# Kernel optimization log

Measured on AMD Instinct MI355X. Metric: run time of the kernel, lower is better.

Reference implementation:

```python
import jax, jax.numpy as jnp
import numpy as np

E = 400000
N = 100000
B = 64
D = 128          # token_dim
H = 128          # hidden_dim
A = 2 * H        # action_dim


def setup_inputs() -> dict:
    key = jax.random.key(0)
    ks = jax.random.split(key, 12)
    inp = {
        "relation_tokens": jax.random.normal(ks[0], (E, D), jnp.float32),
        "node_tokens": jax.random.normal(ks[1], (N, D), jnp.float32),
        "edge_index": jax.random.randint(ks[2], (2, E), 0, N, jnp.int64 if jax.config.jax_enable_x64 else jnp.int32),
        "question_tokens": jax.random.normal(ks[3], (B, D), jnp.float32),
        "edge_batch": jax.random.randint(ks[4], (E,), 0, B, jnp.int64 if jax.config.jax_enable_x64 else jnp.int32),
        # learned params (xavier-like small init); stored as [in, out] for x @ W
        "W_rel": jax.random.normal(ks[5], (D, H), jnp.float32) * 0.05,
        "W_node": jax.random.normal(ks[6], (D, H), jnp.float32) * 0.05,
        "W_qgate": jax.random.normal(ks[7], (D, A), jnp.float32) * 0.05,
        "W_mlp1": jax.random.normal(ks[8], (A, A), jnp.float32) * 0.05,
        "b_mlp1": jnp.zeros((A,), jnp.float32),
        "W_mlp2": jax.random.normal(ks[9], (A, A), jnp.float32) * 0.05,
        "b_mlp2": jnp.zeros((A,), jnp.float32),
    }
    return inp


def reference(relation_tokens, node_tokens, edge_index, question_tokens, edge_batch,
              W_rel, W_node, W_qgate, W_mlp1, b_mlp1, W_mlp2, b_mlp2):
    # TrajectoryAgent.precompute_action_keys (dropout=0 -> identity)
    tail_nodes = edge_index[1]                       # [E]
    tail_tokens = node_tokens[tail_nodes]            # gather -> [E, D]
    q_tokens = question_tokens[edge_batch]           # gather -> [E, D]

    rel_key = relation_tokens @ W_rel                # [E, H]
    node_key = tail_tokens @ W_node                  # [E, H]
    q_gate = jax.nn.sigmoid(q_tokens @ W_qgate)      # [E, 2H]

    action_key = jnp.concatenate((rel_key, node_key), axis=-1) * q_gate  # [E, 2H]

    # action_mlp: Linear -> exact GELU -> Linear (torch nn.GELU default = erf)
    h = jax.nn.gelu(action_key @ W_mlp1 + b_mlp1, approximate=False)
    return h @ W_mlp2 + b_mlp2                       # [E, 2H]
```

## Files before the change

### kernel.cpp

```cpp
#include <hip/hip_runtime.h>

typedef __bf16 bf16;
typedef bf16 bf16x4 __attribute__((ext_vector_type(4)));
typedef bf16 bf16x8 __attribute__((ext_vector_type(8)));
typedef float f32x4 __attribute__((ext_vector_type(4)));

#define WS_PK1   0
#define WS_PK2   32768
#define WS_PK3   98304
#define WS_QG_F  163840

__global__ void prep_weights(const float* __restrict__ Wrel,
                             const float* __restrict__ Wnode,
                             const float* __restrict__ W1,
                             const float* __restrict__ W2,
                             bf16* __restrict__ ws) {
  int id = blockIdx.x * 256 + threadIdx.x;
  if (id < 32768) {
    int cg = id >> 13, rem = id & 8191;
    int kk = rem >> 11;
    int ai = (rem >> 9) & 3;
    int l  = (rem >> 3) & 63;
    int j  = rem & 7;
    int n  = (cg & 1) * 64 + ai * 16 + (l & 15);
    int k  = kk * 32 + (l >> 4) * 8 + j;
    const float* src = (cg >> 1) ? Wnode : Wrel;
    ws[WS_PK1 + id] = (bf16)src[k * 128 + n];
  } else if (id < 98304) {
    int t = id - 32768;
    int cg = t >> 14, rem = t & 16383;
    int kk = rem >> 11;
    int ai = (rem >> 9) & 3;
    int l  = (rem >> 3) & 63;
    int j  = rem & 7;
    int n  = cg * 64 + ai * 16 + (l & 15);
    int k  = kk * 32 + (l >> 4) * 8 + j;
    ws[WS_PK2 + t] = (bf16)W1[k * 256 + n];
  } else if (id < 163840) {
    int t = id - 98304;
    int cg = t >> 14, rem = t & 16383;
    int kk = rem >> 11;
    int ai = (rem >> 9) & 3;
    int l  = (rem >> 3) & 63;
    int j  = rem & 7;
    int n  = cg * 64 + ai * 16 + (l & 15);
    int k  = kk * 32 + (l >> 4) * 8 + j;
    ws[WS_PK3 + t] = (bf16)W2[k * 256 + n];
  }
}

__global__ void prep_qg(const float* __restrict__ question,
                        const float* __restrict__ Wq,
                        float* __restrict__ qgf) {
  int b = blockIdx.x, c = threadIdx.x;
  float s = 0.f;
#pragma unroll 8
  for (int k = 0; k < 128; ++k) s += question[b * 128 + k] * Wq[k * 256 + c];
  qgf[b * 256 + c] = 1.f / (1.f + expf(-s));
}

__device__ __forceinline__ float gelu_fast(float x) {
  float x2 = x * x;
  float p = fmaf(0.0356774081f, x2, 0.7978845608f);
  float y = p * x;
  float e = __expf(2.f * y);
  float r = __builtin_amdgcn_rcpf(e + 1.f);
  float th = 1.f - 2.f * r;
  return 0.5f * x * (1.f + th);
}

__global__ __launch_bounds__(512, 4) void fused_main(
    const float* __restrict__ rel_tok,
    const float* __restrict__ node_tok,
    const int*   __restrict__ tail_idx,
    const int*   __restrict__ ebatch,
    const bf16*  __restrict__ pk1,
    const bf16*  __restrict__ pk2,
    const bf16*  __restrict__ pk3,
    const float* __restrict__ qgf,
    const float* __restrict__ b1,
    const float* __restrict__ b2,
    float* __restrict__ out)
{
  __shared__ char s_buf[65536];
  __shared__ int  s_eb[128];

  const int tid = threadIdx.x;
  const int w   = tid >> 6;
  const int eh  = w >> 2;
  const int cg  = w & 3;
  const int l   = tid & 63;
  const int lo  = l & 15;
  const int hi  = l >> 4;
  const int base = blockIdx.x * 128;

  if (tid < 128) s_eb[tid] = ebatch[base + tid];

  {
    const float4* g = (const float4*)rel_tok + (size_t)base * 32;
#pragma unroll
    for (int i = 0; i < 8; ++i) {
      int idx = tid + i * 512;
      int row = idx >> 5, c4 = idx & 31;
      float4 v = g[idx];
      bf16x4 b; b[0] = (bf16)v.x; b[1] = (bf16)v.y; b[2] = (bf16)v.z; b[3] = (bf16)v.w;
      int off = row * 256 + ((c4 * 8) ^ ((row & 7) << 4));
      *(bf16x4*)(s_buf + off) = b;
    }
#pragma unroll
    for (int i = 0; i < 8; ++i) {
      int idx = tid + i * 512;
      int row = idx >> 5, c4 = idx & 31;
      int tail = tail_idx[base + row];
      float4 v = ((const float4*)node_tok)[(size_t)tail * 32 + c4];
      bf16x4 b; b[0] = (bf16)v.x; b[1] = (bf16)v.y; b[2] = (bf16)v.z; b[3] = (bf16)v.w;
      int off = 32768 + row * 256 + ((c4 * 8) ^ ((row & 7) << 4));
      *(bf16x4*)(s_buf + off) = b;
    }
  }
  __syncthreads();

  const f32x4 zero4 = {0.f, 0.f, 0.f, 0.f};
  const int h1 = cg >> 1;

  f32x4 acc1[4][4];
#pragma unroll
  for (int ai = 0; ai < 4; ++ai)
#pragma unroll
    for (int bj = 0; bj < 4; ++bj) acc1[ai][bj] = zero4;

  {
    const bf16* pw = pk1 + cg * 8192 + l * 8;
#pragma unroll
    for (int kk = 0; kk < 4; ++kk) {
      bf16x8 a[4];
#pragma unroll
      for (int ai = 0; ai < 4; ++ai)
        a[ai] = *(const bf16x8*)(pw + (kk * 4 + ai) * 512);
#pragma unroll
      for (int bj = 0; bj < 4; ++bj) {
        int e = eh * 64 + bj * 16 + lo;
        bf16x8 b = *(const bf16x8*)(s_buf + h1 * 32768 + e * 256 +
                                    ((kk * 64 + hi * 16) ^ ((e & 7) << 4)));
#pragma unroll
        for (int ai = 0; ai < 4; ++ai)
          acc1[ai][bj] = __builtin_amdgcn_mfma_f32_16x16x32_bf16(a[ai], b, acc1[ai][bj], 0, 0, 0);
      }
    }
  }
  __syncthreads();

#pragma unroll
  for (int bj = 0; bj < 4; ++bj) {
    int e = eh * 64 + bj * 16 + lo;
    int qrow = s_eb[e] * 256;
#pragma unroll
    for (int ai = 0; ai < 4; ++ai) {
      int col0 = cg * 64 + ai * 16 + hi * 4;
      float4 g = *(const float4*)(qgf + qrow + col0);
      bf16x4 pk;
      pk[0] = (bf16)(acc1[ai][bj][0] * g.x);
      pk[1] = (bf16)(acc1[ai][bj][1] * g.y);
      pk[2] = (bf16)(acc1[ai][bj][2] * g.z);
      pk[3] = (bf16)(acc1[ai][bj][3] * g.w);
      int off = e * 512 + ((2 * col0) ^ ((e & 7) << 4));
      *(bf16x4*)(s_buf + off) = pk;
    }
  }
  __syncthreads();

  f32x4 acc2[4][4];
#pragma unroll
  for (int ai = 0; ai < 4; ++ai)
#pragma unroll
    for (int bj = 0; bj < 4; ++bj) acc2[ai][bj] = zero4;

  {
    const bf16* pw = pk2 + cg * 16384 + l * 8;
#pragma unroll
    for (int kk = 0; kk < 8; ++kk) {
      bf16x8 a[4];
#pragma unroll
      for (int ai = 0; ai < 4; ++ai)
        a[ai] = *(const bf16x8*)(pw + (kk * 4 + ai) * 512);
#pragma unroll
      for (int bj = 0; bj < 4; ++bj) {
        int e = eh * 64 + bj * 16 + lo;
        bf16x8 b = *(const bf16x8*)(s_buf + e * 512 +
                                    ((kk * 64 + hi * 16) ^ ((e & 7) << 4)));
#pragma unroll
        for (int ai = 0; ai < 4; ++ai)
          acc2[ai][bj] = __builtin_amdgcn_mfma_f32_16x16x32_bf16(a[ai], b, acc2[ai][bj], 0, 0, 0);
      }
    }
  }
  __syncthreads();

  {
    float4 b1v[4];
#pragma unroll
    for (int ai = 0; ai < 4; ++ai)
      b1v[ai] = *(const float4*)(b1 + cg * 64 + ai * 16 + hi * 4);
#pragma unroll
    for (int bj = 0; bj < 4; ++bj) {
      int e = eh * 64 + bj * 16 + lo;
#pragma unroll
      for (int ai = 0; ai < 4; ++ai) {
        int col0 = cg * 64 + ai * 16 + hi * 4;
        bf16x4 pk;
        pk[0] = (bf16)gelu_fast(acc2[ai][bj][0] + b1v[ai].x);
        pk[1] = (bf16)gelu_fast(acc2[ai][bj][1] + b1v[ai].y);
        pk[2] = (bf16)gelu_fast(acc2[ai][bj][2] + b1v[ai].z);
        pk[3] = (bf16)gelu_fast(acc2[ai][bj][3] + b1v[ai].w);
        int off = e * 512 + ((2 * col0) ^ ((e & 7) << 4));
        *(bf16x4*)(s_buf + off) = pk;
      }
    }
  }
  __syncthreads();

  f32x4 acc3[4][4];
#pragma unroll
  for (int ai = 0; ai < 4; ++ai)
#pragma unroll
    for (int bj = 0; bj < 4; ++bj) acc3[ai][bj] = zero4;

  {
    const bf16* pw = pk3 + cg * 16384 + l * 8;
#pragma unroll
    for (int kk = 0; kk < 8; ++kk) {
      bf16x8 a[4];
#pragma unroll
      for (int ai = 0; ai < 4; ++ai)
        a[ai] = *(const bf16x8*)(pw + (kk * 4 + ai) * 512);
#pragma unroll
      for (int bj = 0; bj < 4; ++bj) {
        int e = eh * 64 + bj * 16 + lo;
        bf16x8 b = *(const bf16x8*)(s_buf + e * 512 +
                                    ((kk * 64 + hi * 16) ^ ((e & 7) << 4)));
#pragma unroll
        for (int ai = 0; ai < 4; ++ai)
          acc3[ai][bj] = __builtin_amdgcn_mfma_f32_16x16x32_bf16(a[ai], b, acc3[ai][bj], 0, 0, 0);
      }
    }
  }

  {
    float4 b2v[4];
#pragma unroll
    for (int ai = 0; ai < 4; ++ai)
      b2v[ai] = *(const float4*)(b2 + cg * 64 + ai * 16 + hi * 4);
#pragma unroll
    for (int bj = 0; bj < 4; ++bj) {
      int e = eh * 64 + bj * 16 + lo;
#pragma unroll
      for (int ai = 0; ai < 4; ++ai) {
        int col0 = cg * 64 + ai * 16 + hi * 4;
        float4 o;
        o.x = acc3[ai][bj][0] + b2v[ai].x;
        o.y = acc3[ai][bj][1] + b2v[ai].y;
        o.z = acc3[ai][bj][2] + b2v[ai].z;
        o.w = acc3[ai][bj][3] + b2v[ai].w;
        *(float4*)(out + (size_t)(base + e) * 256 + col0) = o;
      }
    }
  }
}

extern "C" void kernel_launch(void* const* d_in, const int* in_sizes, int n_in,
                              void* d_out, int out_size, void* d_ws, size_t ws_size,
                              hipStream_t stream) {
  const float* rel    = (const float*)d_in[0];
  const float* node   = (const float*)d_in[1];
  const int*   eidx   = (const int*)d_in[2];
  const float* quest  = (const float*)d_in[3];
  const int*   ebat   = (const int*)d_in[4];
  const float* Wrel   = (const float*)d_in[5];
  const float* Wnode  = (const float*)d_in[6];
  const float* Wq     = (const float*)d_in[7];
  const float* W1     = (const float*)d_in[8];
  const float* bias1  = (const float*)d_in[9];
  const float* W2     = (const float*)d_in[10];
  const float* bias2  = (const float*)d_in[11];
  float* outp = (float*)d_out;
  bf16* ws = (bf16*)d_ws;
  float* qgf = (float*)(ws + WS_QG_F);

  const int E = in_sizes[4];

  prep_weights<<<640, 256, 0, stream>>>(Wrel, Wnode, W1, W2, ws);
  prep_qg<<<64, 256, 0, stream>>>(quest, Wq, qgf);
  fused_main<<<E / 128, 512, 0, stream>>>(
      rel, node, eidx + E, ebat,
      ws + WS_PK1, ws + WS_PK2, ws + WS_PK3, qgf,
      bias1, bias2, outp);
}
```

Before: 317.7 us.

## Stream weights into LDS via async global_load_lds double buffer, smaller 64-edge tiles

Weight fragments for all three GEMMs are now staged into a double-buffered LDS region with global_load_lds, two steps ahead, synchronised by manual vmcnt/lgkmcnt waits and raw barriers. Before, each wave read them straight from global memory inside the MFMA loops. The block shrinks to 256 threads and 64 edges with launch bounds (256,2), and the XOR swizzle widens to 16 rows. The question gate is stored in bf16 and prefetched into registers early, together with the biases and edge-batch indices. This is meant to hide weight-load latency behind MFMA work, at the cost of fragile hand-written wait counts and lower occupancy per CU.

```diff
diff --git a/kernel.cpp b/kernel.cpp
--- a/kernel.cpp
+++ b/kernel.cpp
@@ -8,7 +8,7 @@
 #define WS_PK1   0
 #define WS_PK2   32768
 #define WS_PK3   98304
-#define WS_QG_F  163840
+#define WS_QG    163840
 
 __global__ void prep_weights(const float* __restrict__ Wrel,
                              const float* __restrict__ Wnode,
@@ -51,12 +51,12 @@
 
 __global__ void prep_qg(const float* __restrict__ question,
                         const float* __restrict__ Wq,
-                        float* __restrict__ qgf) {
+                        bf16* __restrict__ qg) {
   int b = blockIdx.x, c = threadIdx.x;
   float s = 0.f;
 #pragma unroll 8
   for (int k = 0; k < 128; ++k) s += question[b * 128 + k] * Wq[k * 256 + c];
-  qgf[b * 256 + c] = 1.f / (1.f + expf(-s));
+  qg[b * 256 + c] = (bf16)(1.f / (1.f + expf(-s)));
 }
 
 __device__ __forceinline__ float gelu_fast(float x) {
@@ -69,7 +69,15 @@
   return 0.5f * x * (1.f + th);
 }
 
-__global__ __launch_bounds__(512, 4) void fused_main(
+typedef __attribute__((address_space(1))) const void gq_t;
+typedef __attribute__((address_space(3))) void lq_t;
+#define GLD16(g, s) __builtin_amdgcn_global_load_lds((gq_t*)(g), (lq_t*)(s), 16, 0, 0)
+#define WAIT_VM4()   { asm volatile("s_waitcnt vmcnt(4)" ::: "memory"); __builtin_amdgcn_sched_barrier(0); }
+#define WAIT_VM0()   { asm volatile("s_waitcnt vmcnt(0)" ::: "memory"); __builtin_amdgcn_sched_barrier(0); }
+#define WAIT_LGKM0() { asm volatile("s_waitcnt lgkmcnt(0)" ::: "memory"); __builtin_amdgcn_sched_barrier(0); }
+#define BAR() __builtin_amdgcn_s_barrier()
+
+__global__ __launch_bounds__(256, 2) void fused_main(
     const float* __restrict__ rel_tok,
     const float* __restrict__ node_tok,
     const int*   __restrict__ tail_idx,
@@ -77,51 +85,79 @@
     const bf16*  __restrict__ pk1,
     const bf16*  __restrict__ pk2,
     const bf16*  __restrict__ pk3,
-    const float* __restrict__ qgf,
+    const bf16*  __restrict__ qg,
     const float* __restrict__ b1,
     const float* __restrict__ b2,
     float* __restrict__ out)
 {
-  __shared__ char s_buf[65536];
-  __shared__ int  s_eb[128];
+  __shared__ char s_buf[32768];
+  __shared__ char s_w[32768];
 
   const int tid = threadIdx.x;
-  const int w   = tid >> 6;
-  const int eh  = w >> 2;
-  const int cg  = w & 3;
+  const int cg  = tid >> 6;
   const int l   = tid & 63;
   const int lo  = l & 15;
   const int hi  = l >> 4;
-  const int base = blockIdx.x * 128;
-
-  if (tid < 128) s_eb[tid] = ebatch[base + tid];
+  const int base = blockIdx.x * 64;
+  const int h1  = cg >> 1;
+
+  auto issue_step = [&](int s) {
+    const bf16* g;
+    if (s < 4)       g = pk1 + cg * 8192  + s * 2048;
+    else if (s < 12) g = pk2 + cg * 16384 + (s - 4) * 2048;
+    else             g = pk3 + cg * 16384 + (s - 12) * 2048;
+    g += l * 8;
+    char* d = s_w + (s & 1) * 16384 + cg * 4096;
+#pragma unroll
+    for (int ai = 0; ai < 4; ++ai) GLD16(g + ai * 512, d + ai * 1024);
+  };
+
+  issue_step(0);
+  issue_step(1);
+
+  float4 b1v[4], b2v[4];
+#pragma unroll
+  for (int ai = 0; ai < 4; ++ai) {
+    b1v[ai] = *(const float4*)(b1 + cg * 64 + ai * 16 + hi * 4);
+    b2v[ai] = *(const float4*)(b2 + cg * 64 + ai * 16 + hi * 4);
+  }
+  int ebv[4];
+#pragma unroll
+  for (int bj = 0; bj < 4; ++bj) ebv[bj] = ebatch[base + bj * 16 + lo];
+  bf16x4 gv[4][4];
+#pragma unroll
+  for (int bj = 0; bj < 4; ++bj)
+#pragma unroll
+    for (int ai = 0; ai < 4; ++ai)
+      gv[bj][ai] = *(const bf16x4*)(qg + ebv[bj] * 256 + cg * 64 + ai * 16 + hi * 4);
 
   {
     const float4* g = (const float4*)rel_tok + (size_t)base * 32;
 #pragma unroll
     for (int i = 0; i < 8; ++i) {
-      int idx = tid + i * 512;
+      int idx = tid + i * 256;
       int row = idx >> 5, c4 = idx & 31;
       float4 v = g[idx];
       bf16x4 b; b[0] = (bf16)v.x; b[1] = (bf16)v.y; b[2] = (bf16)v.z; b[3] = (bf16)v.w;
-      int off = row * 256 + ((c4 * 8) ^ ((row & 7) << 4));
+      int off = row * 256 + ((c4 * 8) ^ ((row & 15) << 4));
       *(bf16x4*)(s_buf + off) = b;
     }
 #pragma unroll
     for (int i = 0; i < 8; ++i) {
-      int idx = tid + i * 512;
+      int idx = tid + i * 256;
       int row = idx >> 5, c4 = idx & 31;
       int tail = tail_idx[base + row];
       float4 v = ((const float4*)node_tok)[(size_t)tail * 32 + c4];
       bf16x4 b; b[0] = (bf16)v.x; b[1] = (bf16)v.y; b[2] = (bf16)v.z; b[3] = (bf16)v.w;
-      int off = 32768 + row * 256 + ((c4 * 8) ^ ((row & 7) << 4));
+      int off = 16384 + row * 256 + ((c4 * 8) ^ ((row & 15) << 4));
       *(bf16x4*)(s_buf + off) = b;
     }
   }
-  __syncthreads();
+  WAIT_LGKM0();
+  BAR();
 
   const f32x4 zero4 = {0.f, 0.f, 0.f, 0.f};
-  const int h1 = cg >> 1;
+  const int wb = cg * 4096 + l * 16;
 
   f32x4 acc1[4][4];
 #pragma unroll
@@ -129,45 +165,45 @@
 #pragma unroll
     for (int bj = 0; bj < 4; ++bj) acc1[ai][bj] = zero4;
 
-  {
-    const bf16* pw = pk1 + cg * 8192 + l * 8;
-#pragma unroll
-    for (int kk = 0; kk < 4; ++kk) {
-      bf16x8 a[4];
+#pragma unroll
+  for (int kk = 0; kk < 4; ++kk) {
+    const int s = kk;
+    WAIT_VM4();
+    bf16x8 a[4];
+#pragma unroll
+    for (int ai = 0; ai < 4; ++ai)
+      a[ai] = *(const bf16x8*)(s_w + (s & 1) * 16384 + wb + ai * 1024);
+    WAIT_LGKM0();
+    issue_step(s + 2);
+#pragma unroll
+    for (int bj = 0; bj < 4; ++bj) {
+      int e = bj * 16 + lo;
+      bf16x8 b = *(const bf16x8*)(s_buf + h1 * 16384 + e * 256 +
+                                  ((kk * 64 + hi * 16) ^ ((e & 15) << 4)));
 #pragma unroll
       for (int ai = 0; ai < 4; ++ai)
-        a[ai] = *(const bf16x8*)(pw + (kk * 4 + ai) * 512);
-#pragma unroll
-      for (int bj = 0; bj < 4; ++bj) {
-        int e = eh * 64 + bj * 16 + lo;
-        bf16x8 b = *(const bf16x8*)(s_buf + h1 * 32768 + e * 256 +
-                                    ((kk * 64 + hi * 16) ^ ((e & 7) << 4)));
-#pragma unroll
-        for (int ai = 0; ai < 4; ++ai)
-          acc1[ai][bj] = __builtin_amdgcn_mfma_f32_16x16x32_bf16(a[ai], b, acc1[ai][bj], 0, 0, 0);
-      }
-    }
-  }
-  __syncthreads();
+        acc1[ai][bj] = __builtin_amdgcn_mfma_f32_16x16x32_bf16(a[ai], b, acc1[ai][bj], 0, 0, 0);
+    }
+  }
+  BAR();
 
 #pragma unroll
   for (int bj = 0; bj < 4; ++bj) {
-    int e = eh * 64 + bj * 16 + lo;
-    int qrow = s_eb[e] * 256;
+    int e = bj * 16 + lo;
 #pragma unroll
     for (int ai = 0; ai < 4; ++ai) {
       int col0 = cg * 64 + ai * 16 + hi * 4;
-      float4 g = *(const float4*)(qgf + qrow + col0);
       bf16x4 pk;
-      pk[0] = (bf16)(acc1[ai][bj][0] * g.x);
-      pk[1] = (bf16)(acc1[ai][bj][1] * g.y);
-      pk[2] = (bf16)(acc1[ai][bj][2] * g.z);
-      pk[3] = (bf16)(acc1[ai][bj][3] * g.w);
-      int off = e * 512 + ((2 * col0) ^ ((e & 7) << 4));
+      pk[0] = (bf16)(acc1[ai][bj][0] * (float)gv[bj][ai][0]);
+      pk[1] = (bf16)(acc1[ai][bj][1] * (float)gv[bj][ai][1]);
+      pk[2] = (bf16)(acc1[ai][bj][2] * (float)gv[bj][ai][2]);
+      pk[3] = (bf16)(acc1[ai][bj][3] * (float)gv[bj][ai][3]);
+      int off = e * 512 + ((2 * col0) ^ ((e & 15) << 4));
       *(bf16x4*)(s_buf + off) = pk;
     }
   }
-  __syncthreads();
+  WAIT_LGKM0();
+  BAR();
 
   f32x4 acc2[4][4];
 #pragma unroll
@@ -175,94 +211,85 @@
 #pragma unroll
     for (int bj = 0; bj < 4; ++bj) acc2[ai][bj] = zero4;
 
-  {
-    const bf16* pw = pk2 + cg * 16384 + l * 8;
-#pragma unroll
-    for (int kk = 0; kk < 8; ++kk) {
-      bf16x8 a[4];
+#pragma unroll
+  for (int kk = 0; kk < 8; ++kk) {
+    const int s = 4 + kk;
+    WAIT_VM4();
+    bf16x8 a[4];
+#pragma unroll
+    for (int ai = 0; ai < 4; ++ai)
+      a[ai] = *(const bf16x8*)(s_w + (s & 1) * 16384 + wb + ai * 1024);
+    WAIT_LGKM0();
+    issue_step(s + 2);
+#pragma unroll
+    for (int bj = 0; bj < 4; ++bj) {
+      int e = bj * 16 + lo;
+      bf16x8 b = *(const bf16x8*)(s_buf + e * 512 +
+                                  ((kk * 64 + hi * 16) ^ ((e & 15) << 4)));
 #pragma unroll
       for (int ai = 0; ai < 4; ++ai)
-        a[ai] = *(const bf16x8*)(pw + (kk * 4 + ai) * 512);
-#pragma unroll
-      for (int bj = 0; bj < 4; ++bj) {
-        int e = eh * 64 + bj * 16 + lo;
-        bf16x8 b = *(const bf16x8*)(s_buf + e * 512 +
-                                    ((kk * 64 + hi * 16) ^ ((e & 7) << 4)));
-#pragma unroll
-        for (int ai = 0; ai < 4; ++ai)
-          acc2[ai][bj] = __builtin_amdgcn_mfma_f32_16x16x32_bf16(a[ai], b, acc2[ai][bj], 0, 0, 0);
-      }
-    }
-  }
-  __syncthreads();
-
-  {
-    float4 b1v[4];
+        acc2[ai][bj] = __builtin_amdgcn_mfma_f32_16x16x32_bf16(a[ai], b, acc2[ai][bj], 0, 0, 0);
+    }
+  }
+  BAR();
+
+#pragma unroll
+  for (int bj = 0; bj < 4; ++bj) {
+    int e = bj * 16 + lo;
+#pragma unroll
+    for (int ai = 0; ai < 4; ++ai) {
+      int col0 = cg * 64 + ai * 16 + hi * 4;
+      bf16x4 pk;
+      pk[0] = (bf16)gelu_fast(acc2[ai][bj][0] + b1v[ai].x);
+      pk[1] = (bf16)gelu_fast(acc2[ai][bj][1] + b1v[ai].y);
+      pk[2] = (bf16)gelu_fast(acc2[ai][bj][2] + b1v[ai].z);
+      pk[3] = (bf16)gelu_fast(acc2[ai][bj][3] + b1v[ai].w);
+      int off = e * 512 + ((2 * col0) ^ ((e & 15) << 4));
+      *(bf16x4*)(s_buf + off) = pk;
+    }
+  }
+  WAIT_LGKM0();
+  BAR();
+
+  f32x4 acc3[4][4];
+#pragma unroll
+  for (int ai = 0; ai < 4; ++ai)
+#pragma unroll
+    for (int bj = 0; bj < 4; ++bj) acc3[ai][bj] = zero4;
+
+#pragma unroll
+  for (int kk = 0; kk < 8; ++kk) {
+    const int s = 12 + kk;
+    if (s < 19) { WAIT_VM4(); } else { WAIT_VM0(); }
+    bf16x8 a[4];
 #pragma unroll
     for (int ai = 0; ai < 4; ++ai)
-      b1v[ai] = *(const float4*)(b1 + cg * 64 + ai * 16 + hi * 4);
+      a[ai] = *(const bf16x8*)(s_w + (s & 1) * 16384 + wb + ai * 1024);
+    WAIT_LGKM0();
+    if (s + 2 <= 19) issue_step(s + 2);
 #pragma unroll
     for (int bj = 0; bj < 4; ++bj) {
-      int e = eh * 64 + bj * 16 + lo;
-#pragma unroll
-      for (int ai = 0; ai < 4; ++ai) {
-        int col0 = cg * 64 + ai * 16 + hi * 4;
-        bf16x4 pk;
-        pk[0] = (bf16)gelu_fast(acc2[ai][bj][0] + b1v[ai].x);
-        pk[1] = (bf16)gelu_fast(acc2[ai][bj][1] + b1v[ai].y);
-        pk[2] = (bf16)gelu_fast(acc2[ai][bj][2] + b1v[ai].z);
-        pk[3] = (bf16)gelu_fast(acc2[ai][bj][3] + b1v[ai].w);
-        int off = e * 512 + ((2 * col0) ^ ((e & 7) << 4));
-        *(bf16x4*)(s_buf + off) = pk;
-      }
-    }
-  }
-  __syncthreads();
-
-  f32x4 acc3[4][4];
-#pragma unroll
-  for (int ai = 0; ai < 4; ++ai)
-#pragma unroll
-    for (int bj = 0; bj < 4; ++bj) acc3[ai][bj] = zero4;
-
-  {
-    const bf16* pw = pk3 + cg * 16384 + l * 8;
-#pragma unroll
-    for (int kk = 0; kk < 8; ++kk) {
-      bf16x8 a[4];
+      int e = bj * 16 + lo;
+      bf16x8 b = *(const bf16x8*)(s_buf + e * 512 +
+                                  ((kk * 64 + hi * 16) ^ ((e & 15) << 4)));
 #pragma unroll
       for (int ai = 0; ai < 4; ++ai)
-        a[ai] = *(const bf16x8*)(pw + (kk * 4 + ai) * 512);
-#pragma unroll
-      for (int bj = 0; bj < 4; ++bj) {
-        int e = eh * 64 + bj * 16 + lo;
-        bf16x8 b = *(const bf16x8*)(s_buf + e * 512 +
-                                    ((kk * 64 + hi * 16) ^ ((e & 7) << 4)));
-#pragma unroll
-        for (int ai = 0; ai < 4; ++ai)
-          acc3[ai][bj] = __builtin_amdgcn_mfma_f32_16x16x32_bf16(a[ai], b, acc3[ai][bj], 0, 0, 0);
-      }
-    }
-  }
-
-  {
-    float4 b2v[4];
-#pragma unroll
-    for (int ai = 0; ai < 4; ++ai)
-      b2v[ai] = *(const float4*)(b2 + cg * 64 + ai * 16 + hi * 4);
-#pragma unroll
-    for (int bj = 0; bj < 4; ++bj) {
-      int e = eh * 64 + bj * 16 + lo;
-#pragma unroll
-      for (int ai = 0; ai < 4; ++ai) {
-        int col0 = cg * 64 + ai * 16 + hi * 4;
-        float4 o;
-        o.x = acc3[ai][bj][0] + b2v[ai].x;
-        o.y = acc3[ai][bj][1] + b2v[ai].y;
-        o.z = acc3[ai][bj][2] + b2v[ai].z;
-        o.w = acc3[ai][bj][3] + b2v[ai].w;
-        *(float4*)(out + (size_t)(base + e) * 256 + col0) = o;
-      }
+        acc3[ai][bj] = __builtin_amdgcn_mfma_f32_16x16x32_bf16(a[ai], b, acc3[ai][bj], 0, 0, 0);
+    }
+  }
+
+#pragma unroll
+  for (int bj = 0; bj < 4; ++bj) {
+    int e = bj * 16 + lo;
+#pragma unroll
+    for (int ai = 0; ai < 4; ++ai) {
+      int col0 = cg * 64 + ai * 16 + hi * 4;
+      float4 o;
+      o.x = acc3[ai][bj][0] + b2v[ai].x;
+      o.y = acc3[ai][bj][1] + b2v[ai].y;
+      o.z = acc3[ai][bj][2] + b2v[ai].z;
+      o.w = acc3[ai][bj][3] + b2v[ai].w;
+      *(float4*)(out + (size_t)(base + e) * 256 + col0) = o;
     }
   }
 }
@@ -284,14 +311,13 @@
   const float* bias2  = (const float*)d_in[11];
   float* outp = (float*)d_out;
   bf16* ws = (bf16*)d_ws;
-  float* qgf = (float*)(ws + WS_QG_F);
 
   const int E = in_sizes[4];
 
   prep_weights<<<640, 256, 0, stream>>>(Wrel, Wnode, W1, W2, ws);
-  prep_qg<<<64, 256, 0, stream>>>(quest, Wq, qgf);
-  fused_main<<<E / 128, 512, 0, stream>>>(
+  prep_qg<<<64, 256, 0, stream>>>(quest, Wq, ws + WS_QG);
+  fused_main<<<E / 64, 256, 0, stream>>>(
       rel, node, eidx + E, ebat,
-      ws + WS_PK1, ws + WS_PK2, ws + WS_PK3, qgf,
+      ws + WS_PK1, ws + WS_PK2, ws + WS_PK3, ws + WS_QG,
       bias1, bias2, outp);
 }
```

Result: slower. 479.0 us (+50.8%).
